# Kernel tuning notes

Measured on AMD Instinct MI355X. Metric: run time of the kernel, lower is better.

The kernel has to match this reference:

```python
import jax, jax.numpy as jnp
import numpy as np

DEPTH, LENGTH, WIDTH, NUM_CLASSES = 8, 32, 32, 8
STD_POSITION = 1.0
STD_INTENSITY = 3.0


def setup_inputs() -> dict:
    key = jax.random.key(0)
    k1, k2 = jax.random.split(key)
    patch = jax.random.normal(k1, (DEPTH, LENGTH, WIDTH), dtype=jnp.float32)
    prob = jax.random.uniform(k2, (DEPTH, LENGTH, WIDTH, NUM_CLASSES), dtype=jnp.float32)
    return {"patch": patch, "prob": prob, "k": NUM_CLASSES}


def _dist_weight():
    # Matches torch.meshgrid(arange(depth), arange(length), arange(width)) with 'ij' indexing,
    # then row-major flatten. dist_weight[i,j] = exp(-||pos_i - pos_j||^2 / std_position^2)
    gx, gy, gz = jnp.meshgrid(
        jnp.arange(DEPTH, dtype=jnp.float32),
        jnp.arange(LENGTH, dtype=jnp.float32),
        jnp.arange(WIDTH, dtype=jnp.float32),
        indexing="ij",
    )
    x, y, z = gx.ravel(), gy.ravel(), gz.ravel()  # each [n]
    sq = (
        jnp.square(x[:, None] - x[None, :])
        + jnp.square(y[:, None] - y[None, :])
        + jnp.square(z[:, None] - z[None, :])
    )  # [n, n]
    return jnp.exp(-sq / (STD_POSITION ** 2))


def reference(patch, prob, k):
    n = DEPTH * LENGTH * WIDTH
    f = patch.reshape(-1)  # [n]
    # intensity_weight is .detach()ed in the original -> stop_gradient for faithfulness
    intensity = jax.lax.stop_gradient(
        jnp.exp(-jnp.square((f[:, None] - f[None, :]) / STD_INTENSITY))
    )  # [n, n]
    W = intensity * _dist_weight()  # [n, n]

    P = prob.reshape(n, k)  # row-major flatten matches torch.reshape of prob[:,:,:,t]
    WP = W @ P  # [n, k]
    num = jnp.sum(P * WP, axis=0)            # per-class p^T W p
    den = P.T @ (W @ jnp.ones((n,), W.dtype))  # per-class p^T W 1
    loss = jnp.float32(k) - jnp.sum(num / den)
    return loss.astype(jnp.float32)
```

## Files before the change

kernel.cpp:

```cpp
#include <hip/hip_runtime.h>

#define N        8192
#define NCLS     8
#define WAVES_PB 16
#define TPB      (WAVES_PB * 64)
#define GRID     (N / WAVES_PB)
#define GROUPS   32
#define GPB      (GRID / GROUPS)

#define L1_DW    16384
#define L2_DW    17472
#define BASE_DW  17536

__global__ __launch_bounds__(TPB) void sncut_fused(const float* __restrict__ f,
                                                   const float* __restrict__ P,
                                                   float* __restrict__ ws,
                                                   float* __restrict__ out)
{
    const int tid  = threadIdx.x;
    const int lane = tid & 63;
    const int wave = tid >> 6;
    const int i    = blockIdx.x * WAVES_PB + wave;

    const int zi = i & 31, yi = (i >> 5) & 31, xi = i >> 10;
    const float fi = f[i];

    float v0 = 0.f, v1 = 0.f, v2 = 0.f, v3 = 0.f;
    float v4 = 0.f, v5 = 0.f, v6 = 0.f, v7 = 0.f;
    float vr = 0.f;

    if (lane < 63) {
        const int oy = lane / 9, oz = lane - oy * 9;

        int y0 = yi - 3; y0 = y0 < 0 ? 0 : (y0 > 25 ? 25 : y0);
        int z0 = zi - 4; z0 = z0 < 0 ? 0 : (z0 > 23 ? 23 : z0);
        int x0 = xi - 3; x0 = x0 < 0 ? 0 : (x0 > 1 ? 1 : x0);

        const int yj = y0 + oy, zj = z0 + oz;
        const int dy = yi - yj, dz = zi - zj;
        const float base = (float)(dy * dy + dz * dz);
        const int jcol = (yj << 5) + zj;

        #pragma unroll
        for (int k = 0; k < 7; ++k) {
            const int xj = x0 + k;
            const int dx = xi - xj;
            const int j  = (xj << 10) + jcol;
            const float df  = fi - f[j];
            const float arg = df * df * (1.0f / 9.0f) + (base + (float)(dx * dx));
            const float w   = __expf(-arg);
            const float4 p0 = *reinterpret_cast<const float4*>(P + (size_t)j * NCLS);
            const float4 p1 = *reinterpret_cast<const float4*>(P + (size_t)j * NCLS + 4);
            v0 += w * p0.x; v1 += w * p0.y; v2 += w * p0.z; v3 += w * p0.w;
            v4 += w * p1.x; v5 += w * p1.y; v6 += w * p1.z; v7 += w * p1.w;
            vr += w;
        }
    }

    float vals[9] = {v0, v1, v2, v3, v4, v5, v6, v7, vr};
    #pragma unroll
    for (int v = 0; v < 9; ++v) {
        float x = vals[v];
        #pragma unroll
        for (int off = 32; off > 0; off >>= 1)
            x += __shfl_down(x, off, 64);
        vals[v] = x;
    }

    __shared__ float sh[WAVES_PB][16];
    if (lane == 0) {
        const float4 p0 = *reinterpret_cast<const float4*>(P + (size_t)i * NCLS);
        const float4 p1 = *reinterpret_cast<const float4*>(P + (size_t)i * NCLS + 4);
        sh[wave][0]  = p0.x * vals[0];
        sh[wave][1]  = p0.y * vals[1];
        sh[wave][2]  = p0.z * vals[2];
        sh[wave][3]  = p0.w * vals[3];
        sh[wave][4]  = p1.x * vals[4];
        sh[wave][5]  = p1.y * vals[5];
        sh[wave][6]  = p1.z * vals[6];
        sh[wave][7]  = p1.w * vals[7];
        sh[wave][8]  = p0.x * vals[8];
        sh[wave][9]  = p0.y * vals[8];
        sh[wave][10] = p0.z * vals[8];
        sh[wave][11] = p0.w * vals[8];
        sh[wave][12] = p1.x * vals[8];
        sh[wave][13] = p1.y * vals[8];
        sh[wave][14] = p1.z * vals[8];
        sh[wave][15] = p1.w * vals[8];
    }
    __syncthreads();
    if (tid < 16) {
        float s = 0.f;
        #pragma unroll
        for (int wv = 0; wv < WAVES_PB; ++wv) s += sh[wv][tid];
        __hip_atomic_store(&ws[(size_t)blockIdx.x * 16 + tid], s,
                           __ATOMIC_RELAXED, __HIP_MEMORY_SCOPE_AGENT);
    }

    __shared__ int isLast;
    __syncthreads();
    if (tid == 0) {
        unsigned int* w32 = (unsigned int*)ws;
        const unsigned int base =
            __hip_atomic_load(w32 + BASE_DW, __ATOMIC_RELAXED, __HIP_MEMORY_SCOPE_AGENT);
        const int grp = blockIdx.x >> 4;
        const unsigned int o1 =
            __hip_atomic_fetch_add(w32 + L1_DW + grp * 32, 1u,
                                   __ATOMIC_RELAXED, __HIP_MEMORY_SCOPE_AGENT);
        int last = 0;
        if (((o1 - base) & (unsigned int)(GPB - 1)) == (unsigned int)(GPB - 1)) {
            const unsigned int o2 =
                __hip_atomic_fetch_add(w32 + L2_DW, 1u,
                                       __ATOMIC_RELAXED, __HIP_MEMORY_SCOPE_AGENT);
            last = (((o2 - base) & (unsigned int)(GROUPS - 1)) == (unsigned int)(GROUPS - 1));
        }
        isLast = last;
    }
    __syncthreads();
    if (!isLast) return;

    const int e = tid & 15;
    const int g = tid >> 4;
    float s2 = 0.f;
    #pragma unroll
    for (int m = 0; m < GRID / 64; ++m)
        s2 += __hip_atomic_load(&ws[(size_t)(g + m * 64) * 16 + e],
                                __ATOMIC_RELAXED, __HIP_MEMORY_SCOPE_AGENT);

    __shared__ float acc[64][17];
    acc[g][e] = s2;
    __syncthreads();

    __shared__ float sums[16];
    if (tid < 16) {
        float t = 0.f;
        #pragma unroll
        for (int g2 = 0; g2 < 64; ++g2) t += acc[g2][tid];
        sums[tid] = t;
    }
    __syncthreads();
    if (tid == 0) {
        float loss = (float)NCLS;
        #pragma unroll
        for (int t = 0; t < NCLS; ++t) loss -= sums[t] / sums[NCLS + t];
        out[0] = loss;
    }
}

extern "C" void kernel_launch(void* const* d_in, const int* in_sizes, int n_in,
                              void* d_out, int out_size, void* d_ws, size_t ws_size,
                              hipStream_t stream) {
    const float* f = (const float*)d_in[0];
    const float* P = (const float*)d_in[1];

    sncut_fused<<<GRID, TPB, 0, stream>>>(f, P, (float*)d_ws, (float*)d_out);
}
```

Baseline: 67.05 us.

## Shrink blocks to 4 rows, prefetch neighbor loads, two-level group reduction

Measured after the change: 68.28 us. Within noise of the previous version (+1.8%).

```diff
diff --git a/kernel.cpp b/kernel.cpp
--- a/kernel.cpp
+++ b/kernel.cpp
@@ -2,15 +2,16 @@
 
 #define N        8192
 #define NCLS     8
-#define WAVES_PB 16
-#define TPB      (WAVES_PB * 64)
-#define GRID     (N / WAVES_PB)
-#define GROUPS   32
+#define ROWS_PB  4
+#define TPB      256
+#define GRID     (N / ROWS_PB)
+#define GROUPS   64
 #define GPB      (GRID / GROUPS)
 
-#define L1_DW    16384
-#define L2_DW    17472
-#define BASE_DW  17536
+#define GP_DW    32768
+#define L1_DW    34816
+#define L2_DW    36864
+#define BASE_DW  36992
 
 __global__ __launch_bounds__(TPB) void sncut_fused(const float* __restrict__ f,
                                                    const float* __restrict__ P,
@@ -20,7 +21,7 @@
     const int tid  = threadIdx.x;
     const int lane = tid & 63;
     const int wave = tid >> 6;
-    const int i    = blockIdx.x * WAVES_PB + wave;
+    const int i    = blockIdx.x * ROWS_PB + wave;
 
     const int zi = i & 31, yi = (i >> 5) & 31, xi = i >> 10;
     const float fi = f[i];
@@ -41,19 +42,28 @@
         const float base = (float)(dy * dy + dz * dz);
         const int jcol = (yj << 5) + zj;
 
+        int j = (x0 << 10) + jcol;
+        float  fjA = f[j];
+        float4 p0A = *reinterpret_cast<const float4*>(P + (size_t)j * NCLS);
+        float4 p1A = *reinterpret_cast<const float4*>(P + (size_t)j * NCLS + 4);
+
         #pragma unroll
         for (int k = 0; k < 7; ++k) {
-            const int xj = x0 + k;
-            const int dx = xi - xj;
-            const int j  = (xj << 10) + jcol;
-            const float df  = fi - f[j];
+            float fjN; float4 p0N, p1N;
+            if (k < 6) {
+                const int jn = ((x0 + k + 1) << 10) + jcol;
+                fjN = f[jn];
+                p0N = *reinterpret_cast<const float4*>(P + (size_t)jn * NCLS);
+                p1N = *reinterpret_cast<const float4*>(P + (size_t)jn * NCLS + 4);
+            }
+            const int dx = xi - (x0 + k);
+            const float df  = fi - fjA;
             const float arg = df * df * (1.0f / 9.0f) + (base + (float)(dx * dx));
             const float w   = __expf(-arg);
-            const float4 p0 = *reinterpret_cast<const float4*>(P + (size_t)j * NCLS);
-            const float4 p1 = *reinterpret_cast<const float4*>(P + (size_t)j * NCLS + 4);
-            v0 += w * p0.x; v1 += w * p0.y; v2 += w * p0.z; v3 += w * p0.w;
-            v4 += w * p1.x; v5 += w * p1.y; v6 += w * p1.z; v7 += w * p1.w;
+            v0 += w * p0A.x; v1 += w * p0A.y; v2 += w * p0A.z; v3 += w * p0A.w;
+            v4 += w * p1A.x; v5 += w * p1A.y; v6 += w * p1A.z; v7 += w * p1A.w;
             vr += w;
+            if (k < 6) { fjA = fjN; p0A = p0N; p1A = p1N; }
         }
     }
 
@@ -67,7 +77,7 @@
         vals[v] = x;
     }
 
-    __shared__ float sh[WAVES_PB][16];
+    __shared__ float sh[ROWS_PB][16];
     if (lane == 0) {
         const float4 p0 = *reinterpret_cast<const float4*>(P + (size_t)i * NCLS);
         const float4 p1 = *reinterpret_cast<const float4*>(P + (size_t)i * NCLS + 4);
@@ -90,60 +100,66 @@
     }
     __syncthreads();
     if (tid < 16) {
-        float s = 0.f;
-        #pragma unroll
-        for (int wv = 0; wv < WAVES_PB; ++wv) s += sh[wv][tid];
+        const float s = sh[0][tid] + sh[1][tid] + sh[2][tid] + sh[3][tid];
         __hip_atomic_store(&ws[(size_t)blockIdx.x * 16 + tid], s,
                            __ATOMIC_RELAXED, __HIP_MEMORY_SCOPE_AGENT);
     }
 
-    __shared__ int isLast;
+    __shared__ int flag1;
+    __shared__ unsigned int sbase;
     __syncthreads();
     if (tid == 0) {
         unsigned int* w32 = (unsigned int*)ws;
-        const unsigned int base =
+        const unsigned int pbase =
             __hip_atomic_load(w32 + BASE_DW, __ATOMIC_RELAXED, __HIP_MEMORY_SCOPE_AGENT);
-        const int grp = blockIdx.x >> 4;
+        sbase = pbase;
+        const int grp = blockIdx.x >> 5;
         const unsigned int o1 =
             __hip_atomic_fetch_add(w32 + L1_DW + grp * 32, 1u,
                                    __ATOMIC_RELAXED, __HIP_MEMORY_SCOPE_AGENT);
-        int last = 0;
-        if (((o1 - base) & (unsigned int)(GPB - 1)) == (unsigned int)(GPB - 1)) {
+        flag1 = (((o1 - pbase) & (unsigned int)(GPB - 1)) == (unsigned int)(GPB - 1));
+    }
+    __syncthreads();
+    if (!flag1 || wave != 0) return;
+
+    {
+        const int grp = blockIdx.x >> 5;
+        if (lane < 16) {
+            float gsum = 0.f;
+            #pragma unroll
+            for (int m = 0; m < GPB; ++m)
+                gsum += __hip_atomic_load(&ws[(size_t)(grp * GPB + m) * 16 + lane],
+                                          __ATOMIC_RELAXED, __HIP_MEMORY_SCOPE_AGENT);
+            __hip_atomic_store(&ws[GP_DW + (size_t)grp * 16 + lane], gsum,
+                               __ATOMIC_RELAXED, __HIP_MEMORY_SCOPE_AGENT);
+        }
+        asm volatile("s_waitcnt vmcnt(0)" ::: "memory");
+
+        int gl = 0;
+        if (lane == 0) {
+            unsigned int* w32 = (unsigned int*)ws;
             const unsigned int o2 =
                 __hip_atomic_fetch_add(w32 + L2_DW, 1u,
                                        __ATOMIC_RELAXED, __HIP_MEMORY_SCOPE_AGENT);
-            last = (((o2 - base) & (unsigned int)(GROUPS - 1)) == (unsigned int)(GROUPS - 1));
+            gl = (((o2 - sbase) & (unsigned int)(GROUPS - 1)) == (unsigned int)(GROUPS - 1));
         }
-        isLast = last;
-    }
-    __syncthreads();
-    if (!isLast) return;
+        gl = __shfl(gl, 0, 64);
+        if (!gl) return;
 
-    const int e = tid & 15;
-    const int g = tid >> 4;
-    float s2 = 0.f;
-    #pragma unroll
-    for (int m = 0; m < GRID / 64; ++m)
-        s2 += __hip_atomic_load(&ws[(size_t)(g + m * 64) * 16 + e],
-                                __ATOMIC_RELAXED, __HIP_MEMORY_SCOPE_AGENT);
+        const int e = lane & 15, q = lane >> 4;
+        float s = 0.f;
+        #pragma unroll
+        for (int gg = 0; gg < GROUPS / 4; ++gg)
+            s += __hip_atomic_load(&ws[GP_DW + (size_t)(q + gg * 4) * 16 + e],
+                                   __ATOMIC_RELAXED, __HIP_MEMORY_SCOPE_AGENT);
+        s += __shfl_down(s, 32, 64);
+        s += __shfl_down(s, 16, 64);
 
-    __shared__ float acc[64][17];
-    acc[g][e] = s2;
-    __syncthreads();
-
-    __shared__ float sums[16];
-    if (tid < 16) {
-        float t = 0.f;
-        #pragma unroll
-        for (int g2 = 0; g2 < 64; ++g2) t += acc[g2][tid];
-        sums[tid] = t;
-    }
-    __syncthreads();
-    if (tid == 0) {
-        float loss = (float)NCLS;
-        #pragma unroll
-        for (int t = 0; t < NCLS; ++t) loss -= sums[t] / sums[NCLS + t];
-        out[0] = loss;
+        float r = s / __shfl_down(s, 8, 64);
+        r += __shfl_down(r, 4, 64);
+        r += __shfl_down(r, 2, 64);
+        r += __shfl_down(r, 1, 64);
+        if (lane == 0) out[0] = (float)NCLS - r;
     }
 }
 
```
